# Kernel optimization log

Hardware: AMD Instinct MI355X
Metric: run time of the kernel (lower is better)

The kernel has to match this reference:

```python
import jax, jax.numpy as jnp
import numpy as np

NEG_INF = -jnp.inf  # aggregation identity for the max-plus semifield


def setup_inputs() -> dict:
    key = jax.random.key(0)
    k1, k2, k3 = jax.random.split(key, 3)
    B, C_in, C_out, H, W, M, N = 4, 32, 32, 80, 80, 5, 5
    x = jax.random.normal(k1, (B, C_in, H, W), dtype=jnp.float32)
    w = jax.random.normal(k2, (C_out, C_in, M, N), dtype=jnp.float32) * 0.1
    bias = jax.random.normal(k3, (C_out,), dtype=jnp.float32) * 0.1
    return {"x": x, "w": w, "bias": bias}


def reference(x, w, bias):
    """Max-plus semifield conv: out[b,co,h,w] = bias[co] + sum_ci max_{m,n} (x_pad[b,ci,h+m,w+n] + w[co,ci,m,n]).

    Faithful to SemiConv2d._semi_conv with semifield = (amax, add, -inf, 0),
    but computed with a running max over the MN taps instead of materializing
    the [B, C_out, C_in, M*N, H*W] tensor the torch code builds via unfold.
    """
    B, C_in, H, W = x.shape
    C_out, _, M, N = w.shape
    # padding exactly as in _semi_conv (odd vs even kernel), fill = aggregation identity
    pt, pb = (M // 2, M // 2) if M % 2 else (M // 2 - 1, M // 2)
    pl, pr = (N // 2, N // 2) if N % 2 else (N // 2 - 1, N // 2)
    xp = jnp.pad(x, ((0, 0), (0, 0), (pt, pb), (pl, pr)), constant_values=NEG_INF)
    # running max over the M*N taps (fixed small loop, not a data-dim loop)
    acc = jnp.full((B, C_out, C_in, H, W), NEG_INF, dtype=x.dtype)
    for m in range(M):
        for n in range(N):
            patch = xp[:, :, m:m + H, n:n + W]               # [B, C_in, H, W]
            tap = patch[:, None] + w[None, :, :, m, n, None, None]  # [B, C_out, C_in, H, W]
            acc = jnp.maximum(acc, tap)
    out = jnp.sum(acc, axis=2) + bias[None, :, None, None]   # sum over C_in, add bias
    return out
```

## Files before the change

### kernel.cpp

```cpp
#include <hip/hip_runtime.h>
#include <math.h>

#define CIN  32
#define COUT 32
#define BB   4
#define HH   80
#define WW   80
#define HW   (HH * WW)
#define NOUT (BB * COUT * HW)
#define TH   16
#define XR   20
#define XC   88
#define TILE (XR * XC)
#define NT   320

typedef float v4f __attribute__((ext_vector_type(4)));

__device__ __forceinline__ float max3f(float a, float b, float c) {
    float d;
    asm("v_max3_f32 %0, %1, %2, %3" : "=v"(d) : "v"(a), "v"(b), "v"(c));
    return d;
}

__device__ __forceinline__ void load_lds4(const float* g, float* l) {
    __builtin_amdgcn_global_load_lds(
        (const __attribute__((address_space(1))) void*)g,
        (__attribute__((address_space(3))) void*)l, 4, 0, 0);
}

template<int NP>
__global__ __launch_bounds__(NT, 6) void semiconv_kernel(
    const float* __restrict__ x,
    const float* __restrict__ w,
    const float* __restrict__ bias,
    float* __restrict__ dst)
{
    constexpr int CP = CIN / NP;
    __shared__ __align__(16) float xs0[TILE];
    __shared__ __align__(16) float xs1[TILE];
    __shared__ __align__(16) float wl[CP * 60];

    const int tid = threadIdx.x;
    const int bh  = blockIdx.x;
    const int cp  = blockIdx.y;
    const int zz  = blockIdx.z;
    const int b    = zz / NP;
    const int part = zz % NP;
    const int ci0  = part * CP;
    const int h0   = bh * TH;
    const int co0  = cp * 2;

    for (int idx = tid; idx < CP * 50; idx += NT) {
        int run = idx / (CP * 25);
        int r   = idx % (CP * 25);
        int k = r / 25, t = r % 25, m = t / 5, n = t % 5;
        float v = w[((size_t)(co0 + run) * CIN + ci0) * 25 + r];
        wl[k * 60 + m * 12 + n * 2 + run] = v;
    }

    const int ty = tid / 20, tx = tid % 20, wc = tx * 4;

    int goff[6];
    #pragma unroll
    for (int i = 0; i < 6; ++i) {
        int idx = tid + i * NT;
        int r = idx / XC, c = idx % XC;
        int gr = h0 + r - 2, gc = c - 2;
        bool in = (idx < TILE) && gr >= 0 && gr < HH && gc >= 0 && gc < WW;
        goff[i] = in ? (gr * WW + gc) : -1;
        if (idx < TILE && !in) { xs0[idx] = -INFINITY; xs1[idx] = -INFINITY; }
    }
    const bool has6 = (tid < TILE - 5 * NT);

    const float* xbase = x + (size_t)(b * CIN + ci0) * HW;
    const int wave64 = tid & ~63;

    #pragma unroll
    for (int i = 0; i < 5; ++i)
        if (goff[i] >= 0) load_lds4(xbase + goff[i], xs0 + i * NT + wave64);
    if (has6 && goff[5] >= 0) load_lds4(xbase + goff[5], xs0 + 5 * NT + wave64);

    const float* xnext = xbase + HW;
    float sA[4] = {0.f, 0.f, 0.f, 0.f}, sB[4] = {0.f, 0.f, 0.f, 0.f};
    const int xro = ty * XC + wc;

    __syncthreads();

    auto step = [&](int k, const float* xrd, float* xwr) {
        if (k + 1 < CP) {
            #pragma unroll
            for (int i = 0; i < 5; ++i)
                if (goff[i] >= 0) load_lds4(xnext + goff[i], xwr + i * NT + wave64);
            if (has6 && goff[5] >= 0) load_lds4(xnext + goff[5], xwr + 5 * NT + wave64);
            xnext += HW;
        }
        const float* wk = &wl[k * 60];
        float aA[4] = {-INFINITY, -INFINITY, -INFINITY, -INFINITY};
        float aB[4] = {-INFINITY, -INFINITY, -INFINITY, -INFINITY};
        #pragma unroll
        for (int m = 0; m < 5; ++m) {
            v4f A  = *(const v4f*)(xrd + xro + m * XC);
            v4f C  = *(const v4f*)(xrd + xro + m * XC + 4);
            v4f W0 = *(const v4f*)(wk + m * 12);
            v4f W1 = *(const v4f*)(wk + m * 12 + 4);
            v4f W2 = *(const v4f*)(wk + m * 12 + 8);
            float xr[8] = {A.x, A.y, A.z, A.w, C.x, C.y, C.z, C.w};
            float wa[5] = {W0.x, W0.z, W1.x, W1.z, W2.x};
            float wb[5] = {W0.y, W0.w, W1.y, W1.w, W2.y};
            #pragma unroll
            for (int j = 0; j < 4; ++j) {
                float p0 = xr[j] + wa[0], p1 = xr[j+1] + wa[1], p2 = xr[j+2] + wa[2];
                float p3 = xr[j+3] + wa[3], p4 = xr[j+4] + wa[4];
                aA[j] = max3f(aA[j], max3f(p0, p1, p2), fmaxf(p3, p4));
                p0 = xr[j] + wb[0]; p1 = xr[j+1] + wb[1]; p2 = xr[j+2] + wb[2];
                p3 = xr[j+3] + wb[3]; p4 = xr[j+4] + wb[4];
                aB[j] = max3f(aB[j], max3f(p0, p1, p2), fmaxf(p3, p4));
            }
        }
        #pragma unroll
        for (int j = 0; j < 4; ++j) { sA[j] += aA[j]; sB[j] += aB[j]; }
        __syncthreads();
    };

    #pragma unroll 1
    for (int k = 0; k < CP; k += 2) {
        step(k,     xs0, xs1);
        step(k + 1, xs1, xs0);
    }

    size_t oiA = (((size_t)b * COUT + co0) * HH + (h0 + ty)) * WW + wc;
    size_t oiB = oiA + (size_t)HW;
    v4f rA = {sA[0], sA[1], sA[2], sA[3]};
    v4f rB = {sB[0], sB[1], sB[2], sB[3]};
    float* o = dst;
    if (NP == 1) {
        float bcA = bias[co0], bcB = bias[co0 + 1];
        rA.x += bcA; rA.y += bcA; rA.z += bcA; rA.w += bcA;
        rB.x += bcB; rB.y += bcB; rB.z += bcB; rB.w += bcB;
    } else {
        o += (size_t)part * NOUT;
    }
    *(v4f*)(o + oiA) = rA;
    *(v4f*)(o + oiB) = rB;
}

template<int NP>
__global__ __launch_bounds__(256) void reduceN_kernel(
    const float* __restrict__ ws, const float* __restrict__ bias,
    float* __restrict__ out)
{
    int i4 = blockIdx.x * 256 + threadIdx.x;
    const float4* p = reinterpret_cast<const float4*>(ws);
    float4 r = p[i4];
    #pragma unroll
    for (int q = 1; q < NP; ++q) {
        float4 t = p[i4 + (size_t)q * (NOUT / 4)];
        r.x += t.x; r.y += t.y; r.z += t.z; r.w += t.w;
    }
    int co = (i4 / (HW / 4)) & (COUT - 1);
    float bc = bias[co];
    r.x += bc; r.y += bc; r.z += bc; r.w += bc;
    reinterpret_cast<float4*>(out)[i4] = r;
}

extern "C" void kernel_launch(void* const* d_in, const int* in_sizes, int n_in,
                              void* d_out, int out_size, void* d_ws, size_t ws_size,
                              hipStream_t stream) {
    const float* x    = (const float*)d_in[0];
    const float* w    = (const float*)d_in[1];
    const float* bias = (const float*)d_in[2];
    float* out        = (float*)d_out;

    const size_t need4 = 4ull * NOUT * sizeof(float);
    const size_t need2 = 2ull * NOUT * sizeof(float);

    if (ws_size >= need4) {
        dim3 grid(HH / TH, COUT / 2, BB * 4);
        semiconv_kernel<4><<<grid, NT, 0, stream>>>(x, w, bias, (float*)d_ws);
        reduceN_kernel<4><<<NOUT / 4 / 256, 256, 0, stream>>>((const float*)d_ws, bias, out);
    } else if (ws_size >= need2) {
        dim3 grid(HH / TH, COUT / 2, BB * 2);
        semiconv_kernel<2><<<grid, NT, 0, stream>>>(x, w, bias, (float*)d_ws);
        reduceN_kernel<2><<<NOUT / 4 / 256, 256, 0, stream>>>((const float*)d_ws, bias, out);
    } else {
        dim3 grid(HH / TH, COUT / 2, BB);
        semiconv_kernel<1><<<grid, NT, 0, stream>>>(x, w, bias, out);
    }
}
```

Measured before the change: 38.19 us.

## Compute four output channels per thread and split input channels eight ways

Each block now produces four output channels instead of two, so every x value loaded from LDS is reused across more weight sets. This halves the grid along the output-channel axis. To keep enough blocks, the input-channel split rises from 4 to 8 partial sums when the workspace allows, which doubles the partial-sum buffer traffic and reduce work. Per-thread accumulators grow from 8 to 16 plus 16 partial sums, which raises register pressure under the launch bound.

```diff
diff --git a/kernel.cpp b/kernel.cpp
--- a/kernel.cpp
+++ b/kernel.cpp
@@ -38,24 +38,24 @@
     constexpr int CP = CIN / NP;
     __shared__ __align__(16) float xs0[TILE];
     __shared__ __align__(16) float xs1[TILE];
-    __shared__ __align__(16) float wl[CP * 60];
+    __shared__ __align__(16) float wl[CP * 100];
 
     const int tid = threadIdx.x;
     const int bh  = blockIdx.x;
-    const int cp  = blockIdx.y;
+    const int cq  = blockIdx.y;
     const int zz  = blockIdx.z;
     const int b    = zz / NP;
     const int part = zz % NP;
     const int ci0  = part * CP;
     const int h0   = bh * TH;
-    const int co0  = cp * 2;
-
-    for (int idx = tid; idx < CP * 50; idx += NT) {
-        int run = idx / (CP * 25);
+    const int co0  = cq * 4;
+
+    for (int idx = tid; idx < CP * 100; idx += NT) {
+        int cop = idx / (CP * 25);
         int r   = idx % (CP * 25);
         int k = r / 25, t = r % 25, m = t / 5, n = t % 5;
-        float v = w[((size_t)(co0 + run) * CIN + ci0) * 25 + r];
-        wl[k * 60 + m * 12 + n * 2 + run] = v;
+        wl[k * 100 + m * 20 + n * 4 + cop] =
+            w[((size_t)(co0 + cop) * CIN + ci0) * 25 + r];
     }
 
     const int ty = tid / 20, tx = tid % 20, wc = tx * 4;
@@ -81,7 +81,11 @@
     if (has6 && goff[5] >= 0) load_lds4(xbase + goff[5], xs0 + 5 * NT + wave64);
 
     const float* xnext = xbase + HW;
-    float sA[4] = {0.f, 0.f, 0.f, 0.f}, sB[4] = {0.f, 0.f, 0.f, 0.f};
+    float s[4][4];
+    #pragma unroll
+    for (int c = 0; c < 4; ++c)
+        #pragma unroll
+        for (int j = 0; j < 4; ++j) s[c][j] = 0.f;
     const int xro = ty * XC + wc;
 
     __syncthreads();
@@ -94,31 +98,45 @@
             if (has6 && goff[5] >= 0) load_lds4(xnext + goff[5], xwr + 5 * NT + wave64);
             xnext += HW;
         }
-        const float* wk = &wl[k * 60];
-        float aA[4] = {-INFINITY, -INFINITY, -INFINITY, -INFINITY};
-        float aB[4] = {-INFINITY, -INFINITY, -INFINITY, -INFINITY};
+        const float* wk = &wl[k * 100];
+        float acc[4][4];
+        #pragma unroll
+        for (int c = 0; c < 4; ++c)
+            #pragma unroll
+            for (int j = 0; j < 4; ++j) acc[c][j] = -INFINITY;
+
         #pragma unroll
         for (int m = 0; m < 5; ++m) {
-            v4f A  = *(const v4f*)(xrd + xro + m * XC);
-            v4f C  = *(const v4f*)(xrd + xro + m * XC + 4);
-            v4f W0 = *(const v4f*)(wk + m * 12);
-            v4f W1 = *(const v4f*)(wk + m * 12 + 4);
-            v4f W2 = *(const v4f*)(wk + m * 12 + 8);
+            v4f A = *(const v4f*)(xrd + xro + m * XC);
+            v4f C = *(const v4f*)(xrd + xro + m * XC + 4);
             float xr[8] = {A.x, A.y, A.z, A.w, C.x, C.y, C.z, C.w};
-            float wa[5] = {W0.x, W0.z, W1.x, W1.z, W2.x};
-            float wb[5] = {W0.y, W0.w, W1.y, W1.w, W2.y};
-            #pragma unroll
-            for (int j = 0; j < 4; ++j) {
-                float p0 = xr[j] + wa[0], p1 = xr[j+1] + wa[1], p2 = xr[j+2] + wa[2];
-                float p3 = xr[j+3] + wa[3], p4 = xr[j+4] + wa[4];
-                aA[j] = max3f(aA[j], max3f(p0, p1, p2), fmaxf(p3, p4));
-                p0 = xr[j] + wb[0]; p1 = xr[j+1] + wb[1]; p2 = xr[j+2] + wb[2];
-                p3 = xr[j+3] + wb[3]; p4 = xr[j+4] + wb[4];
-                aB[j] = max3f(aB[j], max3f(p0, p1, p2), fmaxf(p3, p4));
+            v4f W0 = *(const v4f*)(wk + m * 20);
+            v4f W1 = *(const v4f*)(wk + m * 20 + 4);
+            v4f W2 = *(const v4f*)(wk + m * 20 + 8);
+            v4f W3 = *(const v4f*)(wk + m * 20 + 12);
+            v4f W4 = *(const v4f*)(wk + m * 20 + 16);
+            float wn0[4] = {W0.x, W0.y, W0.z, W0.w};
+            float wn1[4] = {W1.x, W1.y, W1.z, W1.w};
+            float wn2[4] = {W2.x, W2.y, W2.z, W2.w};
+            float wn3[4] = {W3.x, W3.y, W3.z, W3.w};
+            float wn4[4] = {W4.x, W4.y, W4.z, W4.w};
+            #pragma unroll
+            for (int c = 0; c < 4; ++c) {
+                #pragma unroll
+                for (int j = 0; j < 4; ++j) {
+                    float p0 = xr[j]     + wn0[c];
+                    float p1 = xr[j + 1] + wn1[c];
+                    float p2 = xr[j + 2] + wn2[c];
+                    float p3 = xr[j + 3] + wn3[c];
+                    float p4 = xr[j + 4] + wn4[c];
+                    acc[c][j] = max3f(acc[c][j], max3f(p0, p1, p2), fmaxf(p3, p4));
+                }
             }
         }
         #pragma unroll
-        for (int j = 0; j < 4; ++j) { sA[j] += aA[j]; sB[j] += aB[j]; }
+        for (int c = 0; c < 4; ++c)
+            #pragma unroll
+            for (int j = 0; j < 4; ++j) s[c][j] += acc[c][j];
         __syncthreads();
     };
 
@@ -128,20 +146,14 @@
         step(k + 1, xs1, xs0);
     }
 
-    size_t oiA = (((size_t)b * COUT + co0) * HH + (h0 + ty)) * WW + wc;
-    size_t oiB = oiA + (size_t)HW;
-    v4f rA = {sA[0], sA[1], sA[2], sA[3]};
-    v4f rB = {sB[0], sB[1], sB[2], sB[3]};
-    float* o = dst;
-    if (NP == 1) {
-        float bcA = bias[co0], bcB = bias[co0 + 1];
-        rA.x += bcA; rA.y += bcA; rA.z += bcA; rA.w += bcA;
-        rB.x += bcB; rB.y += bcB; rB.z += bcB; rB.w += bcB;
-    } else {
-        o += (size_t)part * NOUT;
-    }
-    *(v4f*)(o + oiA) = rA;
-    *(v4f*)(o + oiB) = rB;
+    size_t oi = (((size_t)b * COUT + co0) * HH + (h0 + ty)) * WW + wc;
+    float* o = (NP == 1) ? dst : dst + (size_t)part * NOUT;
+    #pragma unroll
+    for (int c = 0; c < 4; ++c) {
+        float add = (NP == 1) ? bias[co0 + c] : 0.f;
+        v4f r = {s[c][0] + add, s[c][1] + add, s[c][2] + add, s[c][3] + add};
+        *(v4f*)(o + oi + (size_t)c * HW) = r;
+    }
 }
 
 template<int NP>
@@ -171,19 +183,19 @@
     const float* bias = (const float*)d_in[2];
     float* out        = (float*)d_out;
 
+    const size_t need8 = 8ull * NOUT * sizeof(float);
     const size_t need4 = 4ull * NOUT * sizeof(float);
-    const size_t need2 = 2ull * NOUT * sizeof(float);
-
-    if (ws_size >= need4) {
-        dim3 grid(HH / TH, COUT / 2, BB * 4);
+
+    if (ws_size >= need8) {
+        dim3 grid(HH / TH, COUT / 4, BB * 8);
+        semiconv_kernel<8><<<grid, NT, 0, stream>>>(x, w, bias, (float*)d_ws);
+        reduceN_kernel<8><<<NOUT / 4 / 256, 256, 0, stream>>>((const float*)d_ws, bias, out);
+    } else if (ws_size >= need4) {
+        dim3 grid(HH / TH, COUT / 4, BB * 4);
         semiconv_kernel<4><<<grid, NT, 0, stream>>>(x, w, bias, (float*)d_ws);
         reduceN_kernel<4><<<NOUT / 4 / 256, 256, 0, stream>>>((const float*)d_ws, bias, out);
-    } else if (ws_size >= need2) {
-        dim3 grid(HH / TH, COUT / 2, BB * 2);
-        semiconv_kernel<2><<<grid, NT, 0, stream>>>(x, w, bias, (float*)d_ws);
-        reduceN_kernel<2><<<NOUT / 4 / 256, 256, 0, stream>>>((const float*)d_ws, bias, out);
     } else {
-        dim3 grid(HH / TH, COUT / 2, BB);
+        dim3 grid(HH / TH, COUT / 4, BB);
         semiconv_kernel<1><<<grid, NT, 0, stream>>>(x, w, bias, out);
     }
 }
```

New measurement: 44.51 us. 16.5% more time.

## Triple-buffer input tiles with wave-uniform LDS loads and counted waitcnt barriers

Applied to the files above, without the earlier changes.

Replaces the double-buffered x tile with a three-deep LDS ring so tiles k+1 and k+2 are in flight while tile k is computed. Global-to-LDS loads are reorganized per wave, and a dummy load into a trash buffer keeps the outstanding-load count fixed, which allows explicit s_waitcnt vmcnt(6) plus raw s_barrier instead of __syncthreads. It also drops the -inf accumulator init, raises the occupancy hint to 7 blocks per SM, and swaps the NP=1 fallback for a naive kernel. The extra LDS buffer and the tighter launch bounds may pressure occupancy and registers, and the hand-written waitcnt logic is fragile.

```diff
diff --git a/kernel.cpp b/kernel.cpp
--- a/kernel.cpp
+++ b/kernel.cpp
@@ -12,6 +12,7 @@
 #define XR   20
 #define XC   88
 #define TILE (XR * XC)
+#define WSLICE 352
 #define NT   320
 
 typedef float v4f __attribute__((ext_vector_type(4)));
@@ -29,16 +30,16 @@
 }
 
 template<int NP>
-__global__ __launch_bounds__(NT, 6) void semiconv_kernel(
+__global__ __launch_bounds__(NT, 7) void semiconv_kernel(
     const float* __restrict__ x,
     const float* __restrict__ w,
     const float* __restrict__ bias,
     float* __restrict__ dst)
 {
     constexpr int CP = CIN / NP;
-    __shared__ __align__(16) float xs0[TILE];
-    __shared__ __align__(16) float xs1[TILE];
+    __shared__ __align__(16) float xs[3][TILE];
     __shared__ __align__(16) float wl[CP * 60];
+    __shared__ __align__(16) float trash[64];
 
     const int tid = threadIdx.x;
     const int bh  = blockIdx.x;
@@ -50,57 +51,70 @@
     const int h0   = bh * TH;
     const int co0  = cp * 2;
 
+    const int lane = tid & 63;
+    const int wave = tid >> 6;
+    const int wslot = wave * WSLICE;
+
     for (int idx = tid; idx < CP * 50; idx += NT) {
         int run = idx / (CP * 25);
         int r   = idx % (CP * 25);
         int k = r / 25, t = r % 25, m = t / 5, n = t % 5;
-        float v = w[((size_t)(co0 + run) * CIN + ci0) * 25 + r];
-        wl[k * 60 + m * 12 + n * 2 + run] = v;
-    }
-
-    const int ty = tid / 20, tx = tid % 20, wc = tx * 4;
+        wl[k * 60 + m * 12 + n * 2 + run] =
+            w[((size_t)(co0 + run) * CIN + ci0) * 25 + r];
+    }
+    __builtin_amdgcn_sched_barrier(0);
 
     int goff[6];
     #pragma unroll
-    for (int i = 0; i < 6; ++i) {
-        int idx = tid + i * NT;
+    for (int j = 0; j < 6; ++j) {
+        int idx = wslot + j * 64 + lane;
+        bool valid = (j < 5) || (lane < 32);
         int r = idx / XC, c = idx % XC;
         int gr = h0 + r - 2, gc = c - 2;
-        bool in = (idx < TILE) && gr >= 0 && gr < HH && gc >= 0 && gc < WW;
-        goff[i] = in ? (gr * WW + gc) : -1;
-        if (idx < TILE && !in) { xs0[idx] = -INFINITY; xs1[idx] = -INFINITY; }
-    }
-    const bool has6 = (tid < TILE - 5 * NT);
+        bool in = valid && gr >= 0 && gr < HH && gc >= 0 && gc < WW;
+        goff[j] = in ? (gr * WW + gc) : -1;
+        if (valid && !in) {
+            xs[0][idx] = -INFINITY; xs[1][idx] = -INFINITY; xs[2][idx] = -INFINITY;
+        }
+    }
 
     const float* xbase = x + (size_t)(b * CIN + ci0) * HW;
-    const int wave64 = tid & ~63;
+
+    auto issue_tile = [&](int t, int bf) {
+        const float* xp = xbase + (size_t)t * HW;
+        #pragma unroll
+        for (int j = 0; j < 6; ++j) {
+            bool pred = (goff[j] >= 0);
+            if (__any(pred)) {
+                if (pred) load_lds4(xp + goff[j], &xs[bf][wslot + j * 64]);
+            } else {
+                load_lds4(xp, &trash[0]);
+            }
+        }
+    };
+
+    issue_tile(0, 0);
+    issue_tile(1, 1);
+
+    const int ty = tid / 20, tx = tid % 20, wc = tx * 4;
+    const int xro = ty * XC + wc;
+    float sA[4] = {0.f, 0.f, 0.f, 0.f}, sB[4] = {0.f, 0.f, 0.f, 0.f};
+
+    asm volatile("s_waitcnt vmcnt(6) lgkmcnt(0)" ::: "memory");
+    __builtin_amdgcn_s_barrier();
+    __builtin_amdgcn_sched_barrier(0);
 
     #pragma unroll
-    for (int i = 0; i < 5; ++i)
-        if (goff[i] >= 0) load_lds4(xbase + goff[i], xs0 + i * NT + wave64);
-    if (has6 && goff[5] >= 0) load_lds4(xbase + goff[5], xs0 + 5 * NT + wave64);
-
-    const float* xnext = xbase + HW;
-    float sA[4] = {0.f, 0.f, 0.f, 0.f}, sB[4] = {0.f, 0.f, 0.f, 0.f};
-    const int xro = ty * XC + wc;
-
-    __syncthreads();
-
-    auto step = [&](int k, const float* xrd, float* xwr) {
-        if (k + 1 < CP) {
-            #pragma unroll
-            for (int i = 0; i < 5; ++i)
-                if (goff[i] >= 0) load_lds4(xnext + goff[i], xwr + i * NT + wave64);
-            if (has6 && goff[5] >= 0) load_lds4(xnext + goff[5], xwr + 5 * NT + wave64);
-            xnext += HW;
-        }
-        const float* wk = &wl[k * 60];
-        float aA[4] = {-INFINITY, -INFINITY, -INFINITY, -INFINITY};
-        float aB[4] = {-INFINITY, -INFINITY, -INFINITY, -INFINITY};
+    for (int k = 0; k < CP; ++k) {
+        if (k + 2 < CP) issue_tile(k + 2, (k + 2) % 3);
+
+        const float* xk = &xs[k % 3][xro];
+        const float* wk = wl + k * 60;
+        float aA[4], aB[4];
         #pragma unroll
         for (int m = 0; m < 5; ++m) {
-            v4f A  = *(const v4f*)(xrd + xro + m * XC);
-            v4f C  = *(const v4f*)(xrd + xro + m * XC + 4);
+            v4f A  = *(const v4f*)(xk + m * XC);
+            v4f C  = *(const v4f*)(xk + m * XC + 4);
             v4f W0 = *(const v4f*)(wk + m * 12);
             v4f W1 = *(const v4f*)(wk + m * 12 + 4);
             v4f W2 = *(const v4f*)(wk + m * 12 + 8);
@@ -109,23 +123,26 @@
             float wb[5] = {W0.y, W0.w, W1.y, W1.w, W2.y};
             #pragma unroll
             for (int j = 0; j < 4; ++j) {
-                float p0 = xr[j] + wa[0], p1 = xr[j+1] + wa[1], p2 = xr[j+2] + wa[2];
-                float p3 = xr[j+3] + wa[3], p4 = xr[j+4] + wa[4];
-                aA[j] = max3f(aA[j], max3f(p0, p1, p2), fmaxf(p3, p4));
-                p0 = xr[j] + wb[0]; p1 = xr[j+1] + wb[1]; p2 = xr[j+2] + wb[2];
-                p3 = xr[j+3] + wb[3]; p4 = xr[j+4] + wb[4];
-                aB[j] = max3f(aB[j], max3f(p0, p1, p2), fmaxf(p3, p4));
+                float t = max3f(xr[j] + wa[0], xr[j+1] + wa[1], xr[j+2] + wa[2]);
+                float u = fmaxf(xr[j+3] + wa[3], xr[j+4] + wa[4]);
+                aA[j] = (m == 0) ? fmaxf(t, u) : max3f(aA[j], t, u);
+                t = max3f(xr[j] + wb[0], xr[j+1] + wb[1], xr[j+2] + wb[2]);
+                u = fmaxf(xr[j+3] + wb[3], xr[j+4] + wb[4]);
+                aB[j] = (m == 0) ? fmaxf(t, u) : max3f(aB[j], t, u);
             }
         }
         #pragma unroll
         for (int j = 0; j < 4; ++j) { sA[j] += aA[j]; sB[j] += aB[j]; }
-        __syncthreads();
-    };
-
-    #pragma unroll 1
-    for (int k = 0; k < CP; k += 2) {
-        step(k,     xs0, xs1);
-        step(k + 1, xs1, xs0);
+
+        if (k < CP - 2) {
+            asm volatile("s_waitcnt vmcnt(6) lgkmcnt(0)" ::: "memory");
+        } else if (k == CP - 2) {
+            asm volatile("s_waitcnt vmcnt(0) lgkmcnt(0)" ::: "memory");
+        }
+        if (k < CP - 1) {
+            __builtin_amdgcn_s_barrier();
+            __builtin_amdgcn_sched_barrier(0);
+        }
     }
 
     size_t oiA = (((size_t)b * COUT + co0) * HH + (h0 + ty)) * WW + wc;
@@ -163,6 +180,32 @@
     reinterpret_cast<float4*>(out)[i4] = r;
 }
 
+__global__ __launch_bounds__(256) void naive_kernel(
+    const float* __restrict__ x, const float* __restrict__ w,
+    const float* __restrict__ bias, float* __restrict__ out)
+{
+    int o = blockIdx.x * 256 + threadIdx.x;
+    if (o >= NOUT) return;
+    int wcol = o % WW, h = (o / WW) % HH, co = (o / HW) % COUT, b = o / (COUT * HW);
+    float sum = 0.f;
+    for (int ci = 0; ci < CIN; ++ci) {
+        float mx = -INFINITY;
+        for (int m = 0; m < 5; ++m) {
+            int gr = h + m - 2;
+            if (gr < 0 || gr >= HH) continue;
+            for (int n = 0; n < 5; ++n) {
+                int gc = wcol + n - 2;
+                if (gc < 0 || gc >= WW) continue;
+                float v = x[((size_t)(b * CIN + ci)) * HW + gr * WW + gc]
+                        + w[((size_t)(co * CIN + ci)) * 25 + m * 5 + n];
+                mx = fmaxf(mx, v);
+            }
+        }
+        sum += mx;
+    }
+    out[o] = sum + bias[co];
+}
+
 extern "C" void kernel_launch(void* const* d_in, const int* in_sizes, int n_in,
                               void* d_out, int out_size, void* d_ws, size_t ws_size,
                               hipStream_t stream) {
@@ -183,7 +226,6 @@
         semiconv_kernel<2><<<grid, NT, 0, stream>>>(x, w, bias, (float*)d_ws);
         reduceN_kernel<2><<<NOUT / 4 / 256, 256, 0, stream>>>((const float*)d_ws, bias, out);
     } else {
-        dim3 grid(HH / TH, COUT / 2, BB);
-        semiconv_kernel<1><<<grid, NT, 0, stream>>>(x, w, bias, out);
-    }
-}
+        naive_kernel<<<(NOUT + 255) / 256, 256, 0, stream>>>(x, w, bias, out);
+    }
+}
```

New measurement: 40.70 us. 6.6% more time.
